# Kernel optimization log

Hardware: AMD Instinct MI355X
Metric: run time of the kernel (lower is better)

## Reference

```python
import jax, jax.numpy as jnp
import numpy as np

NB_KERNELS = 32
KERNEL_DIM = 16
INPUT_DIM = 1024
BATCH = 1024


def setup_inputs() -> dict:
    key = jax.random.key(0)
    k1, k2 = jax.random.split(key)
    x = jax.random.normal(k1, (BATCH, INPUT_DIM), dtype=jnp.float32)
    # glorot-like scale for the kernel tensor
    W = jax.random.normal(k2, (NB_KERNELS, INPUT_DIM, KERNEL_DIM), dtype=jnp.float32)
    W = W * (1.0 / np.sqrt(INPUT_DIM + KERNEL_DIM))
    return {"x": x, "W": W}


def reference(x, W):
    # activation: (B, K, M) == reshape(dot(x, W))
    act = jnp.einsum('bd,kdm->bkm', x, W)
    # pairwise L1 distances over the kernel_dim axis: (B, K, B)
    # diffs[b,k,m,c] = act[b,k,m] - act[c,k,m]
    diffs = act[:, :, :, None] - jnp.transpose(act, (1, 2, 0))[None, :, :, :]
    abs_diffs = jnp.sum(jnp.abs(diffs), axis=2)          # (B, K, B)
    minibatch_features = jnp.sum(jnp.exp(-abs_diffs), axis=2)  # (B, K)
    return jnp.concatenate([x, minibatch_features], axis=1)
```

## Files before the change

kernel.cpp:

```cpp
#include <hip/hip_runtime.h>
#include <hip/hip_bf16.h>

#define BATCH 1024
#define INPUT_DIM 1024
#define NBK 32
#define KDIM 16

typedef __attribute__((ext_vector_type(8))) short short8;
typedef __attribute__((ext_vector_type(4))) float f32x4;

#define QS8 16.0f
#define EXPC8 (-0.090168443f)

#if __has_builtin(__builtin_amdgcn_sad_u8)
__device__ __forceinline__ unsigned int sadu8(unsigned int a, unsigned int b,
                                              unsigned int acc) {
    return __builtin_amdgcn_sad_u8(a, b, acc);
}
#else
__device__ __forceinline__ unsigned int sadu8(unsigned int a, unsigned int b,
                                              unsigned int acc) {
#pragma unroll
    for (int i = 0; i < 4; ++i) {
        int av = (a >> (8 * i)) & 0xFF, bv = (b >> (8 * i)) & 0xFF;
        int d = av - bv;
        acc += (unsigned int)(d < 0 ? -d : d);
    }
    return acc;
}
#endif

#if __has_builtin(__builtin_amdgcn_exp2f)
__device__ __forceinline__ float fast_exp2(float x) {
    return __builtin_amdgcn_exp2f(x);
}
#else
__device__ __forceinline__ float fast_exp2(float x) { return exp2f(x); }
#endif

__device__ __forceinline__ unsigned int pk_bf16_trunc(float lo, float hi) {
    union { float f; unsigned u; } a, b;
    a.f = lo; b.f = hi;
    return __builtin_amdgcn_perm(b.u, a.u, 0x07060302u);
}

__global__ __launch_bounds__(256) void gemm_k(const float* __restrict__ x,
                                              const float* __restrict__ W,
                                              unsigned char* __restrict__ act2b,
                                              float* __restrict__ out) {
    __shared__ float lds[1536];
    const int bid  = blockIdx.x;
    const int tid  = threadIdx.x;
    const int k    = bid >> 5;
    const int b0   = (bid & 31) * 32;
    const int lane = tid & 63;
    const int w4   = tid >> 6;
    const int m16  = lane & 15;
    const int quad = lane >> 4;

    {
        const int i = bid * 1024 + tid * 4;
        float4 v = *(const float4*)(x + i);
        const int b = i >> 10;
        const int d = i & 1023;
        *(float4*)(out + b * 1056 + d) = v;
    }

    const float* xa0 = x + (b0 + m16) * INPUT_DIM + w4 * 256 + quad * 8;
    const float* xa1 = xa0 + 16 * INPUT_DIM;
    const float* wb  = W + k * (INPUT_DIM * KDIM) + (w4 * 256 + quad * 8) * KDIM + m16;

    f32x4 acc0 = {0.f, 0.f, 0.f, 0.f};
    f32x4 acc1 = {0.f, 0.f, 0.f, 0.f};

#pragma unroll
    for (int s = 0; s < 8; ++s) {
        const float* pa0 = xa0 + s * 32;
        const float* pa1 = xa1 + s * 32;
        const float* pb  = wb + s * 32 * KDIM;
        float4 a0l = *(const float4*)(pa0);
        float4 a0h = *(const float4*)(pa0 + 4);
        float4 a1l = *(const float4*)(pa1);
        float4 a1h = *(const float4*)(pa1 + 4);
        float b0w = pb[0 * KDIM], b1w = pb[1 * KDIM];
        float b2w = pb[2 * KDIM], b3w = pb[3 * KDIM];
        float b4w = pb[4 * KDIM], b5w = pb[5 * KDIM];
        float b6w = pb[6 * KDIM], b7w = pb[7 * KDIM];
        union { unsigned int u[4]; short8 s8; } A0, A1, BV;
        A0.u[0] = pk_bf16_trunc(a0l.x, a0l.y); A0.u[1] = pk_bf16_trunc(a0l.z, a0l.w);
        A0.u[2] = pk_bf16_trunc(a0h.x, a0h.y); A0.u[3] = pk_bf16_trunc(a0h.z, a0h.w);
        A1.u[0] = pk_bf16_trunc(a1l.x, a1l.y); A1.u[1] = pk_bf16_trunc(a1l.z, a1l.w);
        A1.u[2] = pk_bf16_trunc(a1h.x, a1h.y); A1.u[3] = pk_bf16_trunc(a1h.z, a1h.w);
        BV.u[0] = pk_bf16_trunc(b0w, b1w);     BV.u[1] = pk_bf16_trunc(b2w, b3w);
        BV.u[2] = pk_bf16_trunc(b4w, b5w);     BV.u[3] = pk_bf16_trunc(b6w, b7w);
        acc0 = __builtin_amdgcn_mfma_f32_16x16x32_bf16(A0.s8, BV.s8, acc0, 0, 0, 0);
        acc1 = __builtin_amdgcn_mfma_f32_16x16x32_bf16(A1.s8, BV.s8, acc1, 0, 0, 0);
    }

    if (w4 > 0) {
        float* r = &lds[(w4 - 1) * 512 + lane * 8];
        *(float4*)(r)     = make_float4(acc0[0], acc0[1], acc0[2], acc0[3]);
        *(float4*)(r + 4) = make_float4(acc1[0], acc1[1], acc1[2], acc1[3]);
    }
    __syncthreads();
    if (w4 == 0) {
#pragma unroll
        for (int j = 0; j < 3; ++j) {
            const float* r = &lds[j * 512 + lane * 8];
            float4 p0 = *(const float4*)(r);
            float4 p1 = *(const float4*)(r + 4);
            acc0[0] += p0.x; acc0[1] += p0.y; acc0[2] += p0.z; acc0[3] += p0.w;
            acc1[0] += p1.x; acc1[1] += p1.y; acc1[2] += p1.z; acc1[3] += p1.w;
        }
        const int row0 = b0 + quad * 4;
#pragma unroll
        for (int r = 0; r < 4; ++r) {
            float q0 = fminf(fmaxf(acc0[r] * QS8, -127.f), 127.f);
            float q1 = fminf(fmaxf(acc1[r] * QS8, -127.f), 127.f);
            act2b[(k * BATCH + row0 + r) * KDIM + m16] =
                (unsigned char)(128 + (int)rintf(q0));
            act2b[(k * BATCH + row0 + 16 + r) * KDIM + m16] =
                (unsigned char)(128 + (int)rintf(q1));
        }
    }
}

__global__ __launch_bounds__(256) void pairwise_k(const unsigned char* __restrict__ act2b,
                                                  float* __restrict__ part) {
    __shared__ unsigned int cs[32 * 4];
    const int tid = threadIdx.x;
    const int k   = blockIdx.y;
    const int c0  = blockIdx.x * 32;
    const unsigned char* base = act2b + k * (BATCH * KDIM);

    if (tid < 32) ((uint4*)cs)[tid] = ((const uint4*)(base + c0 * KDIM))[tid];

    unsigned int a[4][4];
#pragma unroll
    for (int r = 0; r < 4; ++r) {
        uint4 u = *(const uint4*)(base + (tid + r * 256) * KDIM);
        a[r][0] = u.x; a[r][1] = u.y; a[r][2] = u.z; a[r][3] = u.w;
    }
    __syncthreads();

    float f0 = 0.f, f1 = 0.f, f2 = 0.f, f3 = 0.f;
#pragma unroll 4
    for (int c = 0; c < 32; ++c) {
        uint4 q = *(const uint4*)&cs[c * 4];
        unsigned int cr[4] = {q.x, q.y, q.z, q.w};
        unsigned int s0 = 0u, s1 = 0u, s2 = 0u, s3 = 0u;
#pragma unroll
        for (int j = 0; j < 4; ++j) {
            s0 = sadu8(a[0][j], cr[j], s0);
            s1 = sadu8(a[1][j], cr[j], s1);
            s2 = sadu8(a[2][j], cr[j], s2);
            s3 = sadu8(a[3][j], cr[j], s3);
        }
        f0 += fast_exp2((float)s0 * EXPC8);
        f1 += fast_exp2((float)s1 * EXPC8);
        f2 += fast_exp2((float)s2 * EXPC8);
        f3 += fast_exp2((float)s3 * EXPC8);
    }
    float* p = part + blockIdx.x * (NBK * BATCH) + k * BATCH + tid;
    p[0]   = f0;
    p[256] = f1;
    p[512] = f2;
    p[768] = f3;
}

__global__ __launch_bounds__(256) void combine_k(const float* __restrict__ part,
                                                 float* __restrict__ out) {
    const int t = blockIdx.x * 256 + threadIdx.x;
    const int k = t >> 10;
    const int b = t & 1023;
    float s = 0.f;
#pragma unroll
    for (int i = 0; i < 32; ++i) s += part[i * (NBK * BATCH) + t];
    out[b * 1056 + 1024 + k] = s;
}

extern "C" void kernel_launch(void* const* d_in, const int* in_sizes, int n_in,
                              void* d_out, int out_size, void* d_ws, size_t ws_size,
                              hipStream_t stream) {
    const float* x = (const float*)d_in[0];
    const float* W = (const float*)d_in[1];
    float* out = (float*)d_out;

    unsigned char* act2b = (unsigned char*)d_ws;
    float* part = (float*)((char*)d_ws + 512 * 1024);

    gemm_k<<<1024, 256, 0, stream>>>(x, W, act2b, out);
    pairwise_k<<<dim3(32, 32), 256, 0, stream>>>(act2b, part);
    combine_k<<<128, 256, 0, stream>>>(part, out);
}
```

Measured before the change: 88.01 us.

## Fuse pairwise and combine kernels with in-block reduction over all columns

Replaces the pairwise kernel plus separate combine kernel with one kernel in which each block loads all 1024 quantized columns of a kernel slice into LDS. Eight wave-groups each cover 128 columns for 64 rows, and the partial sums are reduced in shared memory before being written straight to the output. This removes the partial-sum buffer round trip and one kernel launch. In exchange there are fewer register-held rows per thread (less SAD reuse per LDS load), only 512 blocks, and a larger LDS footprint.

```diff
diff --git a/kernel.cpp b/kernel.cpp
--- a/kernel.cpp
+++ b/kernel.cpp
@@ -125,58 +125,45 @@
     }
 }
 
-__global__ __launch_bounds__(256) void pairwise_k(const unsigned char* __restrict__ act2b,
-                                                  float* __restrict__ part) {
-    __shared__ unsigned int cs[32 * 4];
+__global__ __launch_bounds__(512) void pairfull_k(const unsigned char* __restrict__ act2b,
+                                                  float* __restrict__ out) {
+    __shared__ unsigned int cs[1024 * 4];
+    __shared__ float red[8 * 64];
     const int tid = threadIdx.x;
     const int k   = blockIdx.y;
-    const int c0  = blockIdx.x * 32;
+    const int bt  = blockIdx.x;
+    const int row = tid & 63;
+    const int cq  = tid >> 6;
     const unsigned char* base = act2b + k * (BATCH * KDIM);
 
-    if (tid < 32) ((uint4*)cs)[tid] = ((const uint4*)(base + c0 * KDIM))[tid];
+    ((uint4*)cs)[tid]       = ((const uint4*)base)[tid];
+    ((uint4*)cs)[tid + 512] = ((const uint4*)base)[tid + 512];
 
-    unsigned int a[4][4];
-#pragma unroll
-    for (int r = 0; r < 4; ++r) {
-        uint4 u = *(const uint4*)(base + (tid + r * 256) * KDIM);
-        a[r][0] = u.x; a[r][1] = u.y; a[r][2] = u.z; a[r][3] = u.w;
-    }
+    uint4 u = *(const uint4*)(base + (bt * 64 + row) * KDIM);
+    const unsigned int a0 = u.x, a1 = u.y, a2 = u.z, a3 = u.w;
     __syncthreads();
 
-    float f0 = 0.f, f1 = 0.f, f2 = 0.f, f3 = 0.f;
+    float f = 0.f;
+    const unsigned int* cbase = cs + cq * 128 * 4;
 #pragma unroll 4
-    for (int c = 0; c < 32; ++c) {
-        uint4 q = *(const uint4*)&cs[c * 4];
-        unsigned int cr[4] = {q.x, q.y, q.z, q.w};
-        unsigned int s0 = 0u, s1 = 0u, s2 = 0u, s3 = 0u;
+    for (int c = 0; c < 128; ++c) {
+        uint4 q = *(const uint4*)&cbase[c * 4];
+        unsigned int s = 0u;
+        s = sadu8(a0, q.x, s);
+        s = sadu8(a1, q.y, s);
+        s = sadu8(a2, q.z, s);
+        s = sadu8(a3, q.w, s);
+        f += fast_exp2((float)s * EXPC8);
+    }
+
+    red[cq * 64 + row] = f;
+    __syncthreads();
+    if (tid < 64) {
+        float s = 0.f;
 #pragma unroll
-        for (int j = 0; j < 4; ++j) {
-            s0 = sadu8(a[0][j], cr[j], s0);
-            s1 = sadu8(a[1][j], cr[j], s1);
-            s2 = sadu8(a[2][j], cr[j], s2);
-            s3 = sadu8(a[3][j], cr[j], s3);
-        }
-        f0 += fast_exp2((float)s0 * EXPC8);
-        f1 += fast_exp2((float)s1 * EXPC8);
-        f2 += fast_exp2((float)s2 * EXPC8);
-        f3 += fast_exp2((float)s3 * EXPC8);
+        for (int j = 0; j < 8; ++j) s += red[j * 64 + tid];
+        out[(bt * 64 + tid) * 1056 + 1024 + k] = s;
     }
-    float* p = part + blockIdx.x * (NBK * BATCH) + k * BATCH + tid;
-    p[0]   = f0;
-    p[256] = f1;
-    p[512] = f2;
-    p[768] = f3;
-}
-
-__global__ __launch_bounds__(256) void combine_k(const float* __restrict__ part,
-                                                 float* __restrict__ out) {
-    const int t = blockIdx.x * 256 + threadIdx.x;
-    const int k = t >> 10;
-    const int b = t & 1023;
-    float s = 0.f;
-#pragma unroll
-    for (int i = 0; i < 32; ++i) s += part[i * (NBK * BATCH) + t];
-    out[b * 1056 + 1024 + k] = s;
 }
 
 extern "C" void kernel_launch(void* const* d_in, const int* in_sizes, int n_in,
@@ -187,9 +174,7 @@
     float* out = (float*)d_out;
 
     unsigned char* act2b = (unsigned char*)d_ws;
-    float* part = (float*)((char*)d_ws + 512 * 1024);
 
     gemm_k<<<1024, 256, 0, stream>>>(x, W, act2b, out);
-    pairwise_k<<<dim3(32, 32), 256, 0, stream>>>(act2b, part);
-    combine_k<<<128, 256, 0, stream>>>(part, out);
+    pairfull_k<<<dim3(16, 32), 512, 0, stream>>>(act2b, out);
 }
```

Result: faster. 85.06 us (-3.3%).
